# Optimization experiments

Measured on AMD Instinct MI355X. Metric: run time of the kernel, lower is better.

## Reference

```python
import jax, jax.numpy as jnp
import numpy as np

B, T = 1024, 39
NUM_C, NUM_STU, NUM_E, EMB = 123, 100000, 50000, 256
H = 123
IN1 = NUM_C + EMB  # 379


def setup_inputs() -> dict:
    key = jax.random.key(0)
    ks = jax.random.split(key, 32)
    f = lambda k, shp, s: jax.random.normal(k, shp, dtype=jnp.float32) * s
    inp = {}
    inp["q_maritx"] = jax.random.uniform(ks[0], (B, T, NUM_C), dtype=jnp.float32)
    inp["q_maritx_next"] = jax.random.uniform(ks[1], (B, T, NUM_C), dtype=jnp.float32)
    inp["concept"] = jax.random.randint(ks[2], (B, T), 0, NUM_C + 1)
    inp["s_id"] = jax.random.randint(ks[3], (B, 1), 0, NUM_STU + 1)
    inp["e_id"] = jax.random.randint(ks[4], (B, T), 0, NUM_E + 1)
    inp["r"] = jax.random.randint(ks[5], (B, T), 0, 2)
    inp["q_next"] = jax.random.randint(ks[6], (B, T), 0, NUM_E + 1)
    inp["concept_next"] = jax.random.randint(ks[7], (B, T), 0, NUM_C + 1)
    # learned parameters
    inp["emb_problem"] = f(ks[8], (NUM_E + 1, EMB), 1.0)
    inp["student_W"] = f(ks[9], (NUM_STU + 1, NUM_C), 1.0)
    inp["k_diff_W"] = f(ks[10], (NUM_E + 1, NUM_C), 1.0)
    inp["e_disc_W"] = f(ks[11], (NUM_E + 1, 1), 1.0)
    inp["answer_W"] = f(ks[12], (2, EMB), 1.0)
    inp["zz_W"] = f(ks[13], (NUM_C, NUM_C), 0.05)
    inp["zz_b"] = jnp.zeros((NUM_C,), jnp.float32)
    inp["d_t"] = f(ks[14], (1,), 1.0)
    inp["d_e"] = f(ks[15], (1,), 1.0)
    inp["W_ih"] = f(ks[16], (H, IN1), 0.05)
    inp["b_ih"] = jnp.zeros((H,), jnp.float32)
    inp["W_hh"] = f(ks[17], (H, H), 0.05)
    inp["b_hh"] = jnp.zeros((H,), jnp.float32)
    inp["W_tg"] = f(ks[18], (H, 1), 0.05)
    inp["b_tg"] = jnp.zeros((H,), jnp.float32)
    inp["W_z"] = f(ks[19], (H, IN1 + H), 0.05)
    inp["b_z"] = jnp.zeros((H,), jnp.float32)
    inp["W_h"] = f(ks[20], (H, IN1 + H), 0.05)
    inp["b_h"] = jnp.zeros((H,), jnp.float32)
    inp["p1_W"] = f(ks[21], (256, 502), 0.05)
    inp["p1_b"] = jnp.zeros((256,), jnp.float32)
    inp["p2_W"] = f(ks[22], (123, 256), 0.05)
    inp["p2_b"] = jnp.zeros((123,), jnp.float32)
    inp["p3_W"] = f(ks[23], (1, 123), 0.05)
    inp["p3_b"] = jnp.zeros((1,), jnp.float32)
    return inp


def _forward(q_maritx, q_maritx_next, emb_problem, student_W, k_diff_W, e_disc_W,
             answer_W, zz_W, zz_b, d_t, d_e, W_ih, b_ih, W_hh, b_hh, W_tg, b_tg,
             W_z, b_z, W_h, b_h, p1_W, p1_b, p2_W, p2_b, p3_W, p3_b,
             s_id, e_id, r, q_next):
    Bc, Tc = e_id.shape
    e_next_emb = emb_problem[q_next]                       # [B,T,256]
    s_prof = jax.nn.sigmoid(student_W[s_id])               # [B,1,123] (broadcasts vs repeat(1,39,1))
    k_diff = jax.nn.sigmoid(k_diff_W[e_id])                # [B,T,123]
    e_disc = jax.nn.sigmoid(e_disc_W[e_id]) * d_e          # [B,T,1]
    r_emb = answer_W[r]                                    # [B,T,256]
    concept_ab = jnp.einsum('btk,hk->bth', q_maritx, zz_W) + zz_b  # [B,T,123]
    x1 = jnp.concatenate([concept_ab * s_prof, r_emb], axis=-1)    # [B,T,379]
    # --- time-gated RNN: h_t = tanh(W_ih x_t + W_hh h + b) * sigmoid(tg(t)) ---
    Xp = jnp.einsum('bti,hi->bth', x1, W_ih) + b_ih
    tvec = jnp.arange(Tc, dtype=Xp.dtype)[:, None]
    gates = jax.nn.sigmoid(tvec * W_tg[:, 0][None, :] + b_tg)      # [T,123]
    h0 = jnp.zeros((Bc, W_hh.shape[0]), Xp.dtype)

    def step1(h, xs):
        xp, g = xs
        h = jnp.tanh(xp + h @ W_hh.T + b_hh) * g
        return h, h

    _, ys1 = jax.lax.scan(step1, h0, (Xp.transpose(1, 0, 2), gates))
    out_zz = ys1.transpose(1, 0, 2)                        # [B,T,123]
    # --- GRU-like cell (W_r unused in original forward) ---
    input_x1 = e_disc * (d_t * s_prof + (1.0 - d_t) * out_zz - k_diff) * q_maritx
    x2 = jnp.concatenate([input_x1, r_emb], axis=-1)       # [B,T,379]
    nin = x2.shape[-1]
    Wz_x, Wz_h = W_z[:, :nin], W_z[:, nin:]
    Wh_x, Wh_h = W_h[:, :nin], W_h[:, nin:]
    Zx = jnp.einsum('bti,hi->bth', x2, Wz_x) + b_z
    Hx = jnp.einsum('bti,hi->bth', x2, Wh_x) + b_h

    def step2(h, xs):
        zx, hx = xs
        z = jax.nn.sigmoid(zx + h @ Wz_h.T)
        ht = jnp.tanh(hx + h @ Wh_h.T)
        h = (1.0 - z) * h + z * ht
        return h, h

    _, ys2 = jax.lax.scan(step2, h0, (Zx.transpose(1, 0, 2), Hx.transpose(1, 0, 2)))
    outputs = ys2.transpose(1, 0, 2)                       # [B,T,123]
    hcat = jnp.concatenate([outputs, e_next_emb, q_maritx_next], axis=-1)  # [B,T,502]
    o1 = jax.nn.sigmoid(hcat @ p1_W.T + p1_b)  # dropout as identity (deterministic reference)
    o2 = jax.nn.sigmoid(o1 @ p2_W.T + p2_b)
    return jax.nn.sigmoid(o2 @ p3_W.T + p3_b)              # [B,T,1]


def reference(q_maritx, q_maritx_next, emb_problem, student_W, k_diff_W, e_disc_W,
              answer_W, zz_W, zz_b, d_t, d_e, W_ih, b_ih, W_hh, b_hh, W_tg, b_tg,
              W_z, b_z, W_h, b_h, p1_W, p1_b, p2_W, p2_b, p3_W, p3_b,
              concept, s_id, e_id, r, q_next, concept_next):
    # concept / concept_next embeddings are computed but unused in the original output
    return _forward(q_maritx, q_maritx_next, emb_problem, student_W, k_diff_W,
                    e_disc_W, answer_W, zz_W, zz_b, d_t, d_e, W_ih, b_ih, W_hh,
                    b_hh, W_tg, b_tg, W_z, b_z, W_h, b_h, p1_W, p1_b, p2_W,
                    p2_b, p3_W, p3_b, s_id, e_id, r, q_next)
```

## Files before the change

### kernel.cpp

```cpp
#include <hip/hip_runtime.h>
#include <hip/hip_bf16.h>

#define NRB 39936
#define BB 1024
#define TT 39
#define CC 123
#define EMBD 256
#define PCH 136

typedef __attribute__((ext_vector_type(8))) short short8;
typedef __attribute__((ext_vector_type(4))) short shortv4;
typedef __attribute__((ext_vector_type(4))) float floatx4;
typedef unsigned short us;

__device__ __forceinline__ float rcp_(float x){ return __builtin_amdgcn_rcpf(x); }
__device__ __forceinline__ float fsig(float x){ return rcp_(1.f + __expf(-x)); }
__device__ __forceinline__ float ftanh(float x){
  float ax = __builtin_fabsf(x);
  float e = __expf(-2.f*ax);
  float r = (1.f - e) * rcp_(1.f + e);
  return __builtin_copysignf(r, x);
}
__device__ __forceinline__ us f2bf(float x){
  union { float f; unsigned u; } v; v.f = x;
  unsigned r = v.u + 0x7FFFu + ((v.u >> 16) & 1u);
  return (us)(r >> 16);
}
__device__ __forceinline__ us f2bfh(float x){
  __bf16 h = (__bf16)x;
  return __builtin_bit_cast(us, h);
}
__device__ __forceinline__ float bf2f(us u){
  union { unsigned u; float f; } v; v.u = ((unsigned)u) << 16; return v.f;
}

__device__ __forceinline__ void gl_lds16(void* lds, const void* g){
  __builtin_amdgcn_global_load_lds(
      (const __attribute__((address_space(1))) unsigned int*)g,
      (__attribute__((address_space(3))) unsigned int*)lds, 16, 0, 0);
}

#define G_RC 6
#define G_CW 1088
#define G_CAST 2496
#define G_HCAT 1872
#define G_PRE (G_RC + G_CW + G_CAST + G_HCAT)

__global__ __launch_bounds__(256) void k_pre(
    const float* __restrict__ W_ih, const float* __restrict__ W_z,
    const float* __restrict__ W_h, const float* __restrict__ answer_W,
    const float* __restrict__ zz_W, const float* __restrict__ W_hh,
    const float* __restrict__ p1_W, const float* __restrict__ p2_W,
    const float* __restrict__ emb, const int* __restrict__ q_next,
    const float* __restrict__ qmn, const float* __restrict__ q_m,
    float* __restrict__ rtab, us* __restrict__ wts,
    us* __restrict__ p1bf, us* __restrict__ p2bf,
    us* __restrict__ qbf, us* __restrict__ Abf)
{
  const int blk = blockIdx.x, tid = threadIdx.x;
  if (blk < G_RC){
    int which = blk >> 1, j = blk & 1, h = tid;
    if (h >= CC) return;
    const float* W; int stride;
    if (which==0){ W=W_ih; stride=379; } else if (which==1){ W=W_z; stride=502; } else { W=W_h; stride=502; }
    const float* a = answer_W + j*EMBD;
    const float* w = W + (size_t)h*stride + CC;
    float acc = 0.f;
    #pragma unroll 8
    for (int i=0;i<EMBD;i++) acc += w[i]*a[i];
    rtab[(which*2+j)*128 + h] = acc;
    return;
  }
  if (blk < G_RC + G_CW){
    int i = (blk - G_RC)*256 + tid;
    if (i < 7*16384){
      int w = i >> 14, idx = i & 16383, n = idx >> 7, k = idx & 127;
      float v = 0.f;
      if (n < CC && k < CC){
        if      (w==0) v = zz_W[n*CC + k];
        else if (w==1) v = W_ih[n*379 + k];
        else if (w==2) v = W_z [n*502 + k];
        else if (w==3) v = W_h [n*502 + k];
        else if (w==4) v = W_hh[n*CC + k];
        else if (w==5) v = W_z [n*502 + 379 + k];
        else           v = W_h [n*502 + 379 + k];
      }
      wts[i] = f2bf(v);
      return;
    }
    int j = i - 7*16384;
    if (j < 256*512){
      int n = j >> 9, k = j & 511;
      float v;
      if      (k < 379) v = p1_W[n*502 + k + 123];
      else if (k < 384) v = 0.f;
      else if (k < 507) v = p1_W[n*502 + (k - 384)];
      else              v = 0.f;
      p1bf[j] = f2bf(v);
      return;
    }
    j -= 256*512;
    if (j < 128*256){
      int n = j >> 8, k = j & 255;
      p2bf[j] = f2bf(n < CC ? p2_W[n*256 + k] : 0.f);
    }
    return;
  }
  if (blk < G_RC + G_CW + G_CAST){
    const size_t total = (size_t)NRB*128;
    for (size_t i = (size_t)(blk - G_RC - G_CW)*256 + tid; i < total; i += (size_t)G_CAST*256){
      int col = (int)(i & 127); size_t rp = i >> 7;
      int t = (int)(rp >> 10), b = (int)(rp & 1023);
      float v = (col < CC) ? q_m[((size_t)b*TT + t)*CC + col] : 0.f;
      qbf[i] = f2bf(v);
    }
    return;
  }
  {
    const size_t nchunk = (size_t)NRB*48;
    for (size_t c = (size_t)(blk - G_RC - G_CW - G_CAST)*256 + tid; c < nchunk; c += (size_t)G_HCAT*256){
      size_t row = c / 48;
      int c0 = (int)(c - row*48) * 8;
      short8 o;
      if (c0 < 256){
        int qn = q_next[row];
        float4 v0 = *(const float4*)(emb + (size_t)qn*EMBD + c0);
        float4 v1 = *(const float4*)(emb + (size_t)qn*EMBD + c0 + 4);
        o[0]=f2bf(v0.x); o[1]=f2bf(v0.y); o[2]=f2bf(v0.z); o[3]=f2bf(v0.w);
        o[4]=f2bf(v1.x); o[5]=f2bf(v1.y); o[6]=f2bf(v1.z); o[7]=f2bf(v1.w);
      } else {
        int j0 = c0 - 256;
        #pragma unroll
        for (int jj=0;jj<8;jj++){
          int j = j0 + jj;
          o[jj] = (j < CC) ? f2bf(qmn[row*CC + j]) : (short)0;
        }
      }
      *(short8*)(Abf + row*512 + c0) = o;
    }
  }
}

__global__ __launch_bounds__(256) void k_zz_elem(
    const us* __restrict__ X, const us* __restrict__ W,
    const float* __restrict__ zz_b,
    const float* __restrict__ q_m, const int* __restrict__ s_id,
    const int* __restrict__ e_id, const float* __restrict__ student_W,
    const float* __restrict__ k_diff_W, const float* __restrict__ e_disc_W,
    const float* __restrict__ d_t_p, const float* __restrict__ d_e_p,
    us* __restrict__ x1a, us* __restrict__ pre2, us* __restrict__ cqb)
{
  __shared__ __align__(16) us Asl[16][64][8];
  const int tid = threadIdx.x, w = tid >> 6, l = tid & 63, q = l >> 4, r16 = l & 15;
  const int rTile = blockIdx.x*64;
  short8 bfr[2][4];
  #pragma unroll
  for (int nt=0;nt<2;nt++){
    int n = w*32 + nt*16 + r16;
    #pragma unroll
    for (int kt=0;kt<4;kt++)
      bfr[nt][kt] = *(const short8*)(W + (size_t)n*128 + kt*32 + q*8);
  }
  #pragma unroll
  for (int i=0;i<4;i++){
    int seg = i*4 + w;
    gl_lds16(&Asl[seg][l][0], X + (size_t)(rTile+l)*128 + seg*8);
  }
  floatx4 acc[4][2];
  #pragma unroll
  for (int mt=0;mt<4;mt++){
    #pragma unroll
    for (int nt=0;nt<2;nt++){ acc[mt][nt][0]=0.f; acc[mt][nt][1]=0.f; acc[mt][nt][2]=0.f; acc[mt][nt][3]=0.f; }
  }
  __syncthreads();
  #pragma unroll
  for (int kt=0;kt<4;kt++){
    short8 af[4];
    #pragma unroll
    for (int mt=0;mt<4;mt++) af[mt] = *(const short8*)&Asl[kt*4+q][mt*16+r16][0];
    #pragma unroll
    for (int mt=0;mt<4;mt++){
      #pragma unroll
      for (int nt=0;nt<2;nt++)
        acc[mt][nt] = __builtin_amdgcn_mfma_f32_16x16x32_bf16(af[mt], bfr[nt][kt], acc[mt][nt], 0,0,0);
    }
  }
  const float dt = d_t_p[0], de = d_e_p[0];
  float zzb[2]; int colv[2];
  #pragma unroll
  for (int nt=0;nt<2;nt++){
    int col = w*32 + nt*16 + r16; colv[nt] = col;
    zzb[nt] = (col < CC) ? zz_b[col] : 0.f;
  }
  const int t = rTile >> 10;
  #pragma unroll
  for (int mt=0;mt<4;mt++){
    #pragma unroll
    for (int i=0;i<4;i++){
      int row = rTile + mt*16 + q*4 + i;
      int b = row & 1023;
      int g = b*TT + t;
      int btile = b >> 4, r = b & 15;
      int sid = s_id[b];
      int e   = e_id[g];
      float ed = fsig(e_disc_W[e]) * de;
      size_t base = ((size_t)t*64 + btile)*2048;
      #pragma unroll
      for (int nt=0;nt<2;nt++){
        int col = colv[nt];
        float x1v = 0.f, p2v = 0.f, cqv = 0.f;
        if (col < CC){
          float ab = acc[mt][nt][i] + zzb[nt];
          float sp = fsig(student_W[(size_t)sid*CC + col]);
          float kd = fsig(k_diff_W[(size_t)e*CC + col]);
          float qv = q_m[(size_t)g*CC + col];
          x1v = ab*sp;
          p2v = ed*(dt*sp - kd)*qv;
          cqv = ed*(1.f - dt)*qv;
        }
        x1a[base + (size_t)(((col>>5)*64 + ((col>>3)&3)*16 + r)*8) + (col&7)] = f2bf(x1v);
        size_t off = base + (size_t)(((col>>5)*64 + ((r>>2))*16 + (col&15))*8) + ((col>>4)&1)*4 + (r&3);
        pre2[off] = f2bf(p2v);
        cqb[off]  = f2bf(cqv);
      }
    }
  }
}

__global__ __launch_bounds__(256) void k_xp(
    us* __restrict__ x1a, us* __restrict__ qbf, const us* __restrict__ Wih)
{
  const int tid = threadIdx.x, w = tid >> 6, l = tid & 63, q = l >> 4, r16 = l & 15;
  const int rTile = blockIdx.x*64;
  const int tbase = rTile >> 4;
  short8 bfr[2][4];
  #pragma unroll
  for (int nt=0;nt<2;nt++){
    int n = w*32 + nt*16 + r16;
    #pragma unroll
    for (int kt=0;kt<4;kt++)
      bfr[nt][kt] = *(const short8*)(Wih + (size_t)n*128 + kt*32 + q*8);
  }
  floatx4 acc[4][2];
  #pragma unroll
  for (int mt=0;mt<4;mt++){
    #pragma unroll
    for (int nt=0;nt<2;nt++){ acc[mt][nt][0]=0.f; acc[mt][nt][1]=0.f; acc[mt][nt][2]=0.f; acc[mt][nt][3]=0.f; }
  }
  #pragma unroll
  for (int kt=0;kt<4;kt++){
    short8 af[4];
    #pragma unroll
    for (int mt=0;mt<4;mt++)
      af[mt] = *(const short8*)(x1a + (size_t)(tbase+mt)*2048 + (size_t)(kt*64 + q*16 + r16)*8);
    #pragma unroll
    for (int mt=0;mt<4;mt++){
      #pragma unroll
      for (int nt=0;nt<2;nt++)
        acc[mt][nt] = __builtin_amdgcn_mfma_f32_16x16x32_bf16(af[mt], bfr[nt][kt], acc[mt][nt], 0,0,0);
    }
  }
  __syncthreads();
  #pragma unroll
  for (int mt=0;mt<4;mt++){
    #pragma unroll
    for (int nt=0;nt<2;nt++){
      int col = w*32 + nt*16 + r16;
      float* fb = (col < 64) ? (float*)(x1a + (size_t)(tbase+mt)*2048)
                             : (float*)(qbf + (size_t)(tbase+mt)*2048);
      *(floatx4*)(fb + (size_t)(col & 63)*16 + q*4) = acc[mt][nt];
    }
  }
}

__global__ __launch_bounds__(512,1) void k_mid(
    const us* __restrict__ xpa, const us* __restrict__ xpb,
    const us* __restrict__ pre2, const us* __restrict__ cqb,
    const us* __restrict__ Whh,
    const us* __restrict__ Wzx, const us* __restrict__ Whx,
    const us* __restrict__ Wzh, const us* __restrict__ Whh2,
    const float* __restrict__ b_ih, const float* __restrict__ b_z, const float* __restrict__ b_h,
    const float* __restrict__ W_tg, const float* __restrict__ b_tg,
    const float* __restrict__ rtab, const int* __restrict__ r_idx,
    us* __restrict__ Abf)
{
  __shared__ __align__(16) us h1s[2][16*PCH];
  __shared__ __align__(16) us x2s[2][16*PCH];
  __shared__ __align__(16) us h2s[2][16*PCH];
  __shared__ int rint[TT*16];

  const int tid = threadIdx.x, wid = tid >> 6, l = tid & 63, q = l >> 4, r16 = l & 15;
  const bool isA = wid < 4;
  const int gw = wid & 3;
  const int bbase = blockIdx.x*16;
  const int n0 = gw*32 + r16, n1 = n0 + 16;
  const int e7 = r16 & 7;
  const int cb0 = (gw<<2) | (r16>>3);

  short8 w[4][2][4];
  if (isA){
    #pragma unroll
    for (int tt=0;tt<2;tt++){
      const int nn = n0 + tt*16;
      #pragma unroll
      for (int kt=0;kt<4;kt++)
        w[0][tt][kt] = *(const short8*)(Whh + (size_t)nn*128 + kt*32 + q*8);
    }
  } else {
    #pragma unroll
    for (int tt=0;tt<2;tt++){
      const int nn = n0 + tt*16;
      #pragma unroll
      for (int kt=0;kt<4;kt++){
        size_t wofs = (size_t)nn*128 + kt*32 + q*8;
        w[0][tt][kt] = *(const short8*)(Wzx + wofs);
        w[1][tt][kt] = *(const short8*)(Wzh + wofs);
        w[2][tt][kt] = *(const short8*)(Whx + wofs);
        w[3][tt][kt] = *(const short8*)(Whh2 + wofs);
      }
    }
  }

  const bool v0 = n0 < CC, v1 = n1 < CC;
  float ia0[2], ia1[2], ib0[2], ib1[2];
  float wg0=0.f, bg0=0.f, wg1=0.f, bg1=0.f;
  if (isA){
    ia0[0] = v0 ? b_ih[n0] + rtab[n0]     : 0.f;
    ia1[0] = v0 ? b_ih[n0] + rtab[128+n0] : 0.f;
    ia0[1] = v1 ? b_ih[n1] + rtab[n1]     : 0.f;
    ia1[1] = v1 ? b_ih[n1] + rtab[128+n1] : 0.f;
    ib0[0]=0.f; ib1[0]=0.f; ib0[1]=0.f; ib1[1]=0.f;
    wg0 = v0 ? W_tg[n0]:0.f; bg0 = v0 ? b_tg[n0]:0.f;
    wg1 = v1 ? W_tg[n1]:0.f; bg1 = v1 ? b_tg[n1]:0.f;
  } else {
    ia0[0] = v0 ? b_z[n0] + rtab[256+n0] : 0.f;
    ia1[0] = v0 ? b_z[n0] + rtab[384+n0] : 0.f;
    ia0[1] = v1 ? b_z[n1] + rtab[256+n1] : 0.f;
    ia1[1] = v1 ? b_z[n1] + rtab[384+n1] : 0.f;
    ib0[0] = v0 ? b_h[n0] + rtab[512+n0] : 0.f;
    ib1[0] = v0 ? b_h[n0] + rtab[640+n0] : 0.f;
    ib0[1] = v1 ? b_h[n1] + rtab[512+n1] : 0.f;
    ib1[1] = v1 ? b_h[n1] + rtab[640+n1] : 0.f;
  }

  for (int i = tid; i < TT*16; i += 512)
    rint[i] = r_idx[(size_t)(bbase + (i & 15))*TT + (i >> 4)];
  for (int i = tid; i < 16*PCH; i += 512){ h1s[1][i] = 0; h2s[1][i] = 0; }

  const float* xpbase = (gw < 2) ? (const float*)xpa : (const float*)xpb;
  const int xoff = (((gw&1)*32 + r16)*16 + q*4);

  float4 xc0, xc1; short8 pc8, cc8;
  if (isA){
    const float* fb = xpbase + (size_t)blockIdx.x*1024 + xoff;
    xc0 = *(const float4*)fb;
    xc1 = *(const float4*)(fb + 256);
    size_t cofs = (size_t)blockIdx.x*2048 + (size_t)(gw*64 + q*16 + r16)*8;
    pc8 = *(const short8*)(pre2 + cofs);
    cc8 = *(const short8*)(cqb + cofs);
  }
  __syncthreads();

  floatx4 hold0, hold1;
  hold0[0]=0.f; hold0[1]=0.f; hold0[2]=0.f; hold0[3]=0.f;
  hold1[0]=0.f; hold1[1]=0.f; hold1[2]=0.f; hold1[3]=0.f;

  for (int k=0; k<=TT; ++k){
    const int pA = k & 1;
    if (isA){
      float4 xn0, xn1; short8 pcn, ccn;
      if (k+1 < TT){
        size_t tnext = (size_t)(k+1)*64 + blockIdx.x;
        const float* fb = xpbase + tnext*1024 + xoff;
        xn0 = *(const float4*)fb;
        xn1 = *(const float4*)(fb + 256);
        size_t cofs = tnext*2048 + (size_t)(gw*64 + q*16 + r16)*8;
        pcn = *(const short8*)(pre2 + cofs);
        ccn = *(const short8*)(cqb + cofs);
      }
      if (k < TT){
        short8 fr1[4];
        #pragma unroll
        for (int kt=0;kt<4;kt++)
          fr1[kt] = *(const short8*)&h1s[pA^1][r16*PCH + ((kt*4+q)^e7)*8];
        int4 rs = *(const int4*)&rint[k*16 + q*4];
        floatx4 a0, a1;
        a0[0] = (rs.x ? ia1[0] : ia0[0]) + xc0.x;  a1[0] = (rs.x ? ia1[1] : ia0[1]) + xc1.x;
        a0[1] = (rs.y ? ia1[0] : ia0[0]) + xc0.y;  a1[1] = (rs.y ? ia1[1] : ia0[1]) + xc1.y;
        a0[2] = (rs.z ? ia1[0] : ia0[0]) + xc0.z;  a1[2] = (rs.z ? ia1[1] : ia0[1]) + xc1.z;
        a0[3] = (rs.w ? ia1[0] : ia0[0]) + xc0.w;  a1[3] = (rs.w ? ia1[1] : ia0[1]) + xc1.w;
        #pragma unroll
        for (int kt=0;kt<4;kt++){
          a0 = __builtin_amdgcn_mfma_f32_16x16x32_bf16(fr1[kt], w[0][0][kt], a0, 0,0,0);
          a1 = __builtin_amdgcn_mfma_f32_16x16x32_bf16(fr1[kt], w[0][1][kt], a1, 0,0,0);
        }
        float g0 = fsig((float)k*wg0 + bg0);
        float g1 = fsig((float)k*wg1 + bg1);
        #pragma unroll
        for (int i=0;i<4;i++){
          int row = q*4+i;
          int sb0 = row*PCH + ((cb0      ^ (row&7))*8) + e7;
          int sb1 = row*PCH + (((cb0+2)  ^ (row&7))*8) + e7;
          float h1v0 = ftanh(a0[i]) * g0;
          h1s[pA][sb0] = f2bfh(h1v0);
          x2s[pA][sb0] = f2bfh(bf2f((us)pc8[i]) + bf2f((us)cc8[i])*h1v0);
          float h1v1 = ftanh(a1[i]) * g1;
          h1s[pA][sb1] = f2bfh(h1v1);
          x2s[pA][sb1] = f2bfh(bf2f((us)pc8[4+i]) + bf2f((us)cc8[4+i])*h1v1);
        }
      }
      if (k >= 2){
        int row = tid >> 4, cs = tid & 15;
        short8 hv8 = *(const short8*)&h2s[pA][row*PCH + ((cs ^ (row&7))*8)];
        *(short8*)(Abf + ((size_t)(bbase + row)*TT + (k-2))*512 + 384 + cs*8) = hv8;
      }
      if (k+1 < TT){ xc0 = xn0; xc1 = xn1; pc8 = pcn; cc8 = ccn; }
    } else if (k >= 1){
      const int t = k-1, pB = t & 1;
      short8 fx[4], fh[4];
      #pragma unroll
      for (int kt=0;kt<4;kt++){
        int sidx = r16*PCH + ((kt*4+q)^e7)*8;
        fx[kt] = *(const short8*)&x2s[pB][sidx];
        fh[kt] = *(const short8*)&h2s[pB^1][sidx];
      }
      int4 rs = *(const int4*)&rint[t*16 + q*4];
      floatx4 az0, az1, ah0, ah1;
      az0[0] = rs.x ? ia1[0] : ia0[0];  ah0[0] = rs.x ? ib1[0] : ib0[0];
      az0[1] = rs.y ? ia1[0] : ia0[0];  ah0[1] = rs.y ? ib1[0] : ib0[0];
      az0[2] = rs.z ? ia1[0] : ia0[0];  ah0[2] = rs.z ? ib1[0] : ib0[0];
      az0[3] = rs.w ? ia1[0] : ia0[0];  ah0[3] = rs.w ? ib1[0] : ib0[0];
      az1[0] = rs.x ? ia1[1] : ia0[1];  ah1[0] = rs.x ? ib1[1] : ib0[1];
      az1[1] = rs.y ? ia1[1] : ia0[1];  ah1[1] = rs.y ? ib1[1] : ib0[1];
      az1[2] = rs.z ? ia1[1] : ia0[1];  ah1[2] = rs.z ? ib1[1] : ib0[1];
      az1[3] = rs.w ? ia1[1] : ia0[1];  ah1[3] = rs.w ? ib1[1] : ib0[1];
      #pragma unroll
      for (int kt=0;kt<4;kt++){
        az0 = __builtin_amdgcn_mfma_f32_16x16x32_bf16(fx[kt], w[0][0][kt], az0, 0,0,0);
        az0 = __builtin_amdgcn_mfma_f32_16x16x32_bf16(fh[kt], w[1][0][kt], az0, 0,0,0);
        ah0 = __builtin_amdgcn_mfma_f32_16x16x32_bf16(fx[kt], w[2][0][kt], ah0, 0,0,0);
        ah0 = __builtin_amdgcn_mfma_f32_16x16x32_bf16(fh[kt], w[3][0][kt], ah0, 0,0,0);
        az1 = __builtin_amdgcn_mfma_f32_16x16x32_bf16(fx[kt], w[0][1][kt], az1, 0,0,0);
        az1 = __builtin_amdgcn_mfma_f32_16x16x32_bf16(fh[kt], w[1][1][kt], az1, 0,0,0);
        ah1 = __builtin_amdgcn_mfma_f32_16x16x32_bf16(fx[kt], w[2][1][kt], ah1, 0,0,0);
        ah1 = __builtin_amdgcn_mfma_f32_16x16x32_bf16(fh[kt], w[3][1][kt], ah1, 0,0,0);
      }
      #pragma unroll
      for (int i=0;i<4;i++){
        int row = q*4+i;
        int sb0 = row*PCH + ((cb0     ^ (row&7))*8) + e7;
        int sb1 = row*PCH + (((cb0+2) ^ (row&7))*8) + e7;
        float z0  = fsig(az0[i]);
        float th0 = ftanh(ah0[i]);
        hold0[i] += z0*(th0 - hold0[i]);
        h2s[pB][sb0] = f2bfh(hold0[i]);
        float z1  = fsig(az1[i]);
        float th1 = ftanh(ah1[i]);
        hold1[i] += z1*(th1 - hold1[i]);
        h2s[pB][sb1] = f2bfh(hold1[i]);
      }
    }
    __syncthreads();
  }
  if (tid < 256){
    int row = tid >> 4, cs = tid & 15;
    short8 hv8 = *(const short8*)&h2s[(TT-1)&1][row*PCH + ((cs ^ (row&7))*8)];
    *(short8*)(Abf + ((size_t)(bbase + row)*TT + (TT-1))*512 + 384 + cs*8) = hv8;
  }
}

__global__ __launch_bounds__(256) void k_out(
    const us* __restrict__ Abf, const us* __restrict__ p1bf,
    const float* __restrict__ p1_b, const us* __restrict__ p2bf,
    const float* __restrict__ p2_b, const float* __restrict__ p3_W,
    const float* __restrict__ p3_b, float* __restrict__ out)
{
  __shared__ __align__(16) us smem[20480];
  __shared__ float red[64][4];
  us* Asl = smem;
  us* Bsl = smem + 4096;
  us* o1s = smem;
  const int tid = threadIdx.x;
  const int w = tid >> 6, l = tid & 63;
  const int q = l >> 4, r16 = l & 15;
  const int rTile = blockIdx.x * 64;
  floatx4 acc[4][4];
  #pragma unroll
  for (int a=0;a<4;a++){
    #pragma unroll
    for (int b=0;b<4;b++){ acc[a][b][0]=0.f; acc[a][b][1]=0.f; acc[a][b][2]=0.f; acc[a][b][3]=0.f; }
  }
  for (int c = 0; c < 8; c++){
    const int k0 = c*64;
    #pragma unroll
    for (int i=0;i<2;i++){
      int u = i*256 + tid; int seg = u>>6, m = u&63;
      gl_lds16(&Asl[(seg*64 + m)*8], Abf + (size_t)(rTile+m)*512 + k0 + seg*8);
    }
    #pragma unroll
    for (int i=0;i<8;i++){
      int u = i*256 + tid; int seg = u>>8, nn = u&255;
      gl_lds16(&Bsl[(seg*256 + nn)*8], p1bf + (size_t)nn*512 + k0 + seg*8);
    }
    __syncthreads();
    #pragma unroll
    for (int ks=0; ks<2; ks++){
      int seg = ks*4 + q;
      short8 af[4], bfr[4];
      #pragma unroll
      for (int mt=0;mt<4;mt++) af[mt] = *(const short8*)&Asl[(seg*64 + mt*16 + r16)*8];
      #pragma unroll
      for (int nt=0;nt<4;nt++) bfr[nt] = *(const short8*)&Bsl[(seg*256 + w*64 + nt*16 + r16)*8];
      #pragma unroll
      for (int mt=0;mt<4;mt++){
        #pragma unroll
        for (int nt=0;nt<4;nt++)
          acc[mt][nt] = __builtin_amdgcn_mfma_f32_16x16x32_bf16(af[mt], bfr[nt], acc[mt][nt], 0,0,0);
      }
    }
    __syncthreads();
  }
  #pragma unroll
  for (int nt=0;nt<4;nt++){
    int col = w*64 + nt*16 + r16;
    float bb = p1_b[col];
    #pragma unroll
    for (int mt=0;mt<4;mt++){
      #pragma unroll
      for (int i=0;i<4;i++)
        o1s[(mt*16 + q*4 + i)*264 + col] = f2bf(fsig(acc[mt][nt][i] + bb));
    }
  }
  __syncthreads();
  short8 bf2[2][8];
  #pragma unroll
  for (int nt=0;nt<2;nt++){
    int n2 = w*32 + nt*16 + r16;
    #pragma unroll
    for (int kt=0;kt<8;kt++)
      bf2[nt][kt] = *(const short8*)(p2bf + (size_t)n2*256 + kt*32 + q*8);
  }
  floatx4 ac2[4][2];
  #pragma unroll
  for (int mt=0;mt<4;mt++){
    #pragma unroll
    for (int nt=0;nt<2;nt++){ ac2[mt][nt][0]=0.f; ac2[mt][nt][1]=0.f; ac2[mt][nt][2]=0.f; ac2[mt][nt][3]=0.f; }
  }
  #pragma unroll
  for (int kt=0;kt<8;kt++){
    short8 af[4];
    #pragma unroll
    for (int mt=0;mt<4;mt++) af[mt] = *(const short8*)&o1s[(mt*16 + r16)*264 + kt*32 + q*8];
    #pragma unroll
    for (int mt=0;mt<4;mt++){
      #pragma unroll
      for (int nt=0;nt<2;nt++)
        ac2[mt][nt] = __builtin_amdgcn_mfma_f32_16x16x32_bf16(af[mt], bf2[nt][kt], ac2[mt][nt], 0,0,0);
    }
  }
  const int n0 = w*32 + r16, n1 = n0 + 16;
  const float pb0 = (n0<CC)? p2_b[n0]:0.f, pb1 = (n1<CC)? p2_b[n1]:0.f;
  const float p30 = (n0<CC)? p3_W[n0]:0.f, p31 = (n1<CC)? p3_W[n1]:0.f;
  #pragma unroll
  for (int mt=0;mt<4;mt++){
    #pragma unroll
    for (int i=0;i<4;i++){
      float s = fsig(ac2[mt][0][i]+pb0)*p30 + fsig(ac2[mt][1][i]+pb1)*p31;
      s += __shfl_xor(s,1,16); s += __shfl_xor(s,2,16);
      s += __shfl_xor(s,4,16); s += __shfl_xor(s,8,16);
      if (r16==0) red[mt*16 + q*4 + i][w] = s;
    }
  }
  __syncthreads();
  if (tid < 64){
    float o = red[tid][0]+red[tid][1]+red[tid][2]+red[tid][3] + p3_b[0];
    out[rTile + tid] = fsig(o);
  }
}

extern "C" void kernel_launch(void* const* d_in, const int* in_sizes, int n_in,
                              void* d_out, int out_size, void* d_ws, size_t ws_size,
                              hipStream_t stream) {
  const float* q_m       = (const float*)d_in[0];
  const float* q_m_next  = (const float*)d_in[1];
  const int*   s_id      = (const int*)d_in[3];
  const int*   e_id      = (const int*)d_in[4];
  const int*   r_idx     = (const int*)d_in[5];
  const int*   q_next    = (const int*)d_in[6];
  const float* emb_problem = (const float*)d_in[8];
  const float* student_W = (const float*)d_in[9];
  const float* k_diff_W  = (const float*)d_in[10];
  const float* e_disc_W  = (const float*)d_in[11];
  const float* answer_W  = (const float*)d_in[12];
  const float* zz_W      = (const float*)d_in[13];
  const float* zz_b      = (const float*)d_in[14];
  const float* d_t       = (const float*)d_in[15];
  const float* d_e       = (const float*)d_in[16];
  const float* W_ih      = (const float*)d_in[17];
  const float* b_ih      = (const float*)d_in[18];
  const float* W_hh      = (const float*)d_in[19];
  const float* W_tg      = (const float*)d_in[21];
  const float* b_tg      = (const float*)d_in[22];
  const float* W_z       = (const float*)d_in[23];
  const float* b_z       = (const float*)d_in[24];
  const float* W_h       = (const float*)d_in[25];
  const float* b_h       = (const float*)d_in[26];
  const float* p1_W      = (const float*)d_in[27];
  const float* p1_b      = (const float*)d_in[28];
  const float* p2_W      = (const float*)d_in[29];
  const float* p2_b      = (const float*)d_in[30];
  const float* p3_W      = (const float*)d_in[31];
  const float* p3_b      = (const float*)d_in[32];

  float* ws   = (float*)d_ws;
  float* rtab = ws;
  us* qbf  = (us*)(ws + 1024);
  us* x1a  = qbf  + (size_t)NRB*128;
  us* pre2 = x1a  + (size_t)NRB*128;
  us* cqb  = pre2 + (size_t)NRB*128;
  us* Abf  = cqb  + (size_t)NRB*128;
  us* wts  = Abf  + (size_t)NRB*512;
  us* p1bf = wts  + 7*16384;
  us* p2bf = p1bf + 256*512;

  const us* zzWbf  = wts + 0*16384;
  const us* Wih123 = wts + 1*16384;
  const us* Wz123  = wts + 2*16384;
  const us* Wh123  = wts + 3*16384;
  const us* Whhbf  = wts + 4*16384;
  const us* Wzhbf  = wts + 5*16384;
  const us* Whh2bf = wts + 6*16384;

  hipLaunchKernelGGL(k_pre, dim3(G_PRE), dim3(256), 0, stream,
                     W_ih, W_z, W_h, answer_W, zz_W, W_hh, p1_W, p2_W,
                     emb_problem, q_next, q_m_next, q_m,
                     rtab, wts, p1bf, p2bf, qbf, Abf);
  hipLaunchKernelGGL(k_zz_elem, dim3(NRB/64), dim3(256), 0, stream,
                     qbf, zzWbf, zz_b, q_m, s_id, e_id, student_W, k_diff_W,
                     e_disc_W, d_t, d_e, x1a, pre2, cqb);
  hipLaunchKernelGGL(k_xp, dim3(NRB/64), dim3(256), 0, stream,
                     x1a, qbf, Wih123);
  hipLaunchKernelGGL(k_mid, dim3(BB/16), dim3(512), 0, stream,
                     x1a, qbf, pre2, cqb, Whhbf, Wz123, Wh123, Wzhbf, Whh2bf,
                     b_ih, b_z, b_h, W_tg, b_tg, rtab, r_idx, Abf);
  hipLaunchKernelGGL(k_out, dim3(NRB/64), dim3(256), 0, stream,
                     Abf, p1bf, p1_b, p2bf, p2_b, p3_W, p3_b, (float*)d_out);
}
```

Before: 383.0 us.

## Fuse input projection into zz kernel via LDS and drop k_mid swizzle

The separate k_xp kernel is folded into k_zz_elem. The bf16 x1 tile now stays in shared memory and is multiplied by W_ih right away, instead of being written to global memory and read back by a second launch. This removes one kernel launch and a global round trip for x1, at the cost of more registers for a second set of weight fragments and an extra barrier. Separately, k_mid's XOR-swizzled LDS indexing is replaced by plain padded row-major indexing. That saves integer address arithmetic but may bring back some LDS bank conflicts.

```diff
diff --git a/kernel.cpp b/kernel.cpp
--- a/kernel.cpp
+++ b/kernel.cpp
@@ -143,23 +143,29 @@
 
 __global__ __launch_bounds__(256) void k_zz_elem(
     const us* __restrict__ X, const us* __restrict__ W,
+    const us* __restrict__ Wih,
     const float* __restrict__ zz_b,
     const float* __restrict__ q_m, const int* __restrict__ s_id,
     const int* __restrict__ e_id, const float* __restrict__ student_W,
     const float* __restrict__ k_diff_W, const float* __restrict__ e_disc_W,
     const float* __restrict__ d_t_p, const float* __restrict__ d_e_p,
-    us* __restrict__ x1a, us* __restrict__ pre2, us* __restrict__ cqb)
+    us* __restrict__ xpa, us* __restrict__ xpb,
+    us* __restrict__ pre2, us* __restrict__ cqb)
 {
   __shared__ __align__(16) us Asl[16][64][8];
+  us* x1l = &Asl[0][0][0];
   const int tid = threadIdx.x, w = tid >> 6, l = tid & 63, q = l >> 4, r16 = l & 15;
   const int rTile = blockIdx.x*64;
-  short8 bfr[2][4];
+  const int tbase = rTile >> 4;
+  short8 bfr[2][4], bfr2[2][4];
   #pragma unroll
   for (int nt=0;nt<2;nt++){
     int n = w*32 + nt*16 + r16;
     #pragma unroll
-    for (int kt=0;kt<4;kt++)
-      bfr[nt][kt] = *(const short8*)(W + (size_t)n*128 + kt*32 + q*8);
+    for (int kt=0;kt<4;kt++){
+      bfr[nt][kt]  = *(const short8*)(W   + (size_t)n*128 + kt*32 + q*8);
+      bfr2[nt][kt] = *(const short8*)(Wih + (size_t)n*128 + kt*32 + q*8);
+    }
   }
   #pragma unroll
   for (int i=0;i<4;i++){
@@ -185,6 +191,7 @@
         acc[mt][nt] = __builtin_amdgcn_mfma_f32_16x16x32_bf16(af[mt], bfr[nt][kt], acc[mt][nt], 0,0,0);
     }
   }
+  __syncthreads();
   const float dt = d_t_p[0], de = d_e_p[0];
   float zzb[2]; int colv[2];
   #pragma unroll
@@ -218,57 +225,41 @@
           p2v = ed*(dt*sp - kd)*qv;
           cqv = ed*(1.f - dt)*qv;
         }
-        x1a[base + (size_t)(((col>>5)*64 + ((col>>3)&3)*16 + r)*8) + (col&7)] = f2bf(x1v);
+        x1l[mt*2048 + (w*64 + (nt*2 + (r16>>3))*16 + (q*4+i))*8 + (r16&7)] = f2bf(x1v);
         size_t off = base + (size_t)(((col>>5)*64 + ((r>>2))*16 + (col&15))*8) + ((col>>4)&1)*4 + (r&3);
         pre2[off] = f2bf(p2v);
         cqb[off]  = f2bf(cqv);
       }
     }
   }
-}
-
-__global__ __launch_bounds__(256) void k_xp(
-    us* __restrict__ x1a, us* __restrict__ qbf, const us* __restrict__ Wih)
-{
-  const int tid = threadIdx.x, w = tid >> 6, l = tid & 63, q = l >> 4, r16 = l & 15;
-  const int rTile = blockIdx.x*64;
-  const int tbase = rTile >> 4;
-  short8 bfr[2][4];
-  #pragma unroll
-  for (int nt=0;nt<2;nt++){
-    int n = w*32 + nt*16 + r16;
-    #pragma unroll
-    for (int kt=0;kt<4;kt++)
-      bfr[nt][kt] = *(const short8*)(Wih + (size_t)n*128 + kt*32 + q*8);
-  }
-  floatx4 acc[4][2];
+  __syncthreads();
+  floatx4 ac2[4][2];
   #pragma unroll
   for (int mt=0;mt<4;mt++){
     #pragma unroll
-    for (int nt=0;nt<2;nt++){ acc[mt][nt][0]=0.f; acc[mt][nt][1]=0.f; acc[mt][nt][2]=0.f; acc[mt][nt][3]=0.f; }
+    for (int nt=0;nt<2;nt++){ ac2[mt][nt][0]=0.f; ac2[mt][nt][1]=0.f; ac2[mt][nt][2]=0.f; ac2[mt][nt][3]=0.f; }
   }
   #pragma unroll
   for (int kt=0;kt<4;kt++){
     short8 af[4];
     #pragma unroll
     for (int mt=0;mt<4;mt++)
-      af[mt] = *(const short8*)(x1a + (size_t)(tbase+mt)*2048 + (size_t)(kt*64 + q*16 + r16)*8);
+      af[mt] = *(const short8*)&x1l[mt*2048 + (size_t)(kt*64 + q*16 + r16)*8];
     #pragma unroll
     for (int mt=0;mt<4;mt++){
       #pragma unroll
       for (int nt=0;nt<2;nt++)
-        acc[mt][nt] = __builtin_amdgcn_mfma_f32_16x16x32_bf16(af[mt], bfr[nt][kt], acc[mt][nt], 0,0,0);
-    }
-  }
-  __syncthreads();
+        ac2[mt][nt] = __builtin_amdgcn_mfma_f32_16x16x32_bf16(af[mt], bfr2[nt][kt], ac2[mt][nt], 0,0,0);
+    }
+  }
   #pragma unroll
   for (int mt=0;mt<4;mt++){
     #pragma unroll
     for (int nt=0;nt<2;nt++){
       int col = w*32 + nt*16 + r16;
-      float* fb = (col < 64) ? (float*)(x1a + (size_t)(tbase+mt)*2048)
-                             : (float*)(qbf + (size_t)(tbase+mt)*2048);
-      *(floatx4*)(fb + (size_t)(col & 63)*16 + q*4) = acc[mt][nt];
+      float* fb = (col < 64) ? (float*)(xpa + (size_t)(tbase+mt)*2048)
+                             : (float*)(xpb + (size_t)(tbase+mt)*2048);
+      *(floatx4*)(fb + (size_t)(col & 63)*16 + q*4) = ac2[mt][nt];
     }
   }
 }
@@ -294,8 +285,6 @@
   const int gw = wid & 3;
   const int bbase = blockIdx.x*16;
   const int n0 = gw*32 + r16, n1 = n0 + 16;
-  const int e7 = r16 & 7;
-  const int cb0 = (gw<<2) | (r16>>3);
 
   short8 w[4][2][4];
   if (isA){
@@ -382,7 +371,7 @@
         short8 fr1[4];
         #pragma unroll
         for (int kt=0;kt<4;kt++)
-          fr1[kt] = *(const short8*)&h1s[pA^1][r16*PCH + ((kt*4+q)^e7)*8];
+          fr1[kt] = *(const short8*)&h1s[pA^1][r16*PCH + kt*32 + q*8];
         int4 rs = *(const int4*)&rint[k*16 + q*4];
         floatx4 a0, a1;
         a0[0] = (rs.x ? ia1[0] : ia0[0]) + xc0.x;  a1[0] = (rs.x ? ia1[1] : ia0[1]) + xc1.x;
@@ -398,20 +387,17 @@
         float g1 = fsig((float)k*wg1 + bg1);
         #pragma unroll
         for (int i=0;i<4;i++){
-          int row = q*4+i;
-          int sb0 = row*PCH + ((cb0      ^ (row&7))*8) + e7;
-          int sb1 = row*PCH + (((cb0+2)  ^ (row&7))*8) + e7;
           float h1v0 = ftanh(a0[i]) * g0;
-          h1s[pA][sb0] = f2bfh(h1v0);
-          x2s[pA][sb0] = f2bfh(bf2f((us)pc8[i]) + bf2f((us)cc8[i])*h1v0);
+          h1s[pA][(q*4+i)*PCH + n0] = f2bfh(h1v0);
+          x2s[pA][(q*4+i)*PCH + n0] = f2bfh(bf2f((us)pc8[i]) + bf2f((us)cc8[i])*h1v0);
           float h1v1 = ftanh(a1[i]) * g1;
-          h1s[pA][sb1] = f2bfh(h1v1);
-          x2s[pA][sb1] = f2bfh(bf2f((us)pc8[4+i]) + bf2f((us)cc8[4+i])*h1v1);
+          h1s[pA][(q*4+i)*PCH + n1] = f2bfh(h1v1);
+          x2s[pA][(q*4+i)*PCH + n1] = f2bfh(bf2f((us)pc8[4+i]) + bf2f((us)cc8[4+i])*h1v1);
         }
       }
       if (k >= 2){
         int row = tid >> 4, cs = tid & 15;
-        short8 hv8 = *(const short8*)&h2s[pA][row*PCH + ((cs ^ (row&7))*8)];
+        short8 hv8 = *(const short8*)&h2s[pA][row*PCH + cs*8];
         *(short8*)(Abf + ((size_t)(bbase + row)*TT + (k-2))*512 + 384 + cs*8) = hv8;
       }
       if (k+1 < TT){ xc0 = xn0; xc1 = xn1; pc8 = pcn; cc8 = ccn; }
@@ -420,7 +406,7 @@
       short8 fx[4], fh[4];
       #pragma unroll
       for (int kt=0;kt<4;kt++){
-        int sidx = r16*PCH + ((kt*4+q)^e7)*8;
+        int sidx = r16*PCH + kt*32 + q*8;
         fx[kt] = *(const short8*)&x2s[pB][sidx];
         fh[kt] = *(const short8*)&h2s[pB^1][sidx];
       }
@@ -447,24 +433,21 @@
       }
       #pragma unroll
       for (int i=0;i<4;i++){
-        int row = q*4+i;
-        int sb0 = row*PCH + ((cb0     ^ (row&7))*8) + e7;
-        int sb1 = row*PCH + (((cb0+2) ^ (row&7))*8) + e7;
         float z0  = fsig(az0[i]);
         float th0 = ftanh(ah0[i]);
         hold0[i] += z0*(th0 - hold0[i]);
-        h2s[pB][sb0] = f2bfh(hold0[i]);
+        h2s[pB][(q*4+i)*PCH + n0] = f2bfh(hold0[i]);
         float z1  = fsig(az1[i]);
         float th1 = ftanh(ah1[i]);
         hold1[i] += z1*(th1 - hold1[i]);
-        h2s[pB][sb1] = f2bfh(hold1[i]);
+        h2s[pB][(q*4+i)*PCH + n1] = f2bfh(hold1[i]);
       }
     }
     __syncthreads();
   }
   if (tid < 256){
     int row = tid >> 4, cs = tid & 15;
-    short8 hv8 = *(const short8*)&h2s[(TT-1)&1][row*PCH + ((cs ^ (row&7))*8)];
+    short8 hv8 = *(const short8*)&h2s[(TT-1)&1][row*PCH + cs*8];
     *(short8*)(Abf + ((size_t)(bbase + row)*TT + (TT-1))*512 + 384 + cs*8) = hv8;
   }
 }
@@ -636,10 +619,8 @@
                      emb_problem, q_next, q_m_next, q_m,
                      rtab, wts, p1bf, p2bf, qbf, Abf);
   hipLaunchKernelGGL(k_zz_elem, dim3(NRB/64), dim3(256), 0, stream,
-                     qbf, zzWbf, zz_b, q_m, s_id, e_id, student_W, k_diff_W,
-                     e_disc_W, d_t, d_e, x1a, pre2, cqb);
-  hipLaunchKernelGGL(k_xp, dim3(NRB/64), dim3(256), 0, stream,
-                     x1a, qbf, Wih123);
+                     qbf, zzWbf, Wih123, zz_b, q_m, s_id, e_id, student_W, k_diff_W,
+                     e_disc_W, d_t, d_e, x1a, qbf, pre2, cqb);
   hipLaunchKernelGGL(k_mid, dim3(BB/16), dim3(512), 0, stream,
                      x1a, qbf, pre2, cqb, Whhbf, Wz123, Wh123, Wzhbf, Whh2bf,
                      b_ih, b_z, b_h, W_tg, b_tg, rtab, r_idx, Abf);
```

Result: faster. 374.1 us (-2.3%).
